# Kernel tuning notes

Hardware: AMD Instinct MI355X
Metric: run time of the kernel (lower is better)

## Reference

```python
import jax, jax.numpy as jnp
import numpy as np

NUM_HEADS = 4
WS = 3


def setup_inputs() -> dict:
    key = jax.random.key(0)
    k1, k2, k3 = jax.random.split(key, 3)
    B, Hs, Ws_, C = 16, 96, 96, 256
    x = jax.random.normal(k1, (B, Hs * Ws_, C), dtype=jnp.float32)
    # torch nn.Linear weights: [out_features, in_features]
    Wqkv = jax.random.normal(k2, (3 * C, C), dtype=jnp.float32) * (1.0 / np.sqrt(C))
    Wproj = jax.random.normal(k3, (C, C), dtype=jnp.float32) * (1.0 / np.sqrt(C))
    return {"x": x, "Wqkv": Wqkv, "Wproj": Wproj, "H": Hs, "W": Ws_}


def reference(x, Wqkv, Wproj, H, W):
    B, N, C = x.shape
    ws = WS
    nh = NUM_HEADS
    hd = C // nh
    scale = hd ** -0.5

    pad_h = (ws - H % ws) % ws
    pad_w = (ws - W % ws) % ws
    xg = x.reshape(B, H, W, C)
    if pad_h > 0 or pad_w > 0:
        xg = jnp.pad(xg, ((0, 0), (0, pad_h), (0, pad_w), (0, 0)))
    H_pad, W_pad = H + pad_h, W + pad_w
    nWh, nWw = H_pad // ws, W_pad // ws
    Bw = B * nWh * nWw

    # window partition: [B, nWh, ws, nWw, ws, C] -> [Bw, ws*ws, C]
    xw = xg.reshape(B, nWh, ws, nWw, ws, C).transpose(0, 1, 3, 2, 4, 5)
    xw = xw.reshape(Bw, ws * ws, C)

    # qkv projection (Linear, no bias): x @ W^T
    qkv = xw @ Wqkv.T                                   # [Bw, 9, 3C]
    qkv = qkv.reshape(Bw, ws * ws, 3, nh, hd).transpose(2, 0, 3, 1, 4)
    q, k, v = qkv[0], qkv[1], qkv[2]                    # [Bw, nh, 9, hd]

    attn = jnp.einsum("bhqd,bhkd->bhqk", q, k) * scale  # [Bw, nh, 9, 9]
    attn = jax.nn.softmax(attn, axis=-1)
    out = jnp.einsum("bhqk,bhkd->bhqd", attn, v)        # [Bw, nh, 9, hd]
    out = out.transpose(0, 2, 1, 3).reshape(Bw, ws * ws, C)
    out = out @ Wproj.T

    # window unpartition
    out = out.reshape(B, nWh, nWw, ws, ws, C).transpose(0, 1, 3, 2, 4, 5)
    out = out.reshape(B, H_pad, W_pad, C)
    if pad_h > 0 or pad_w > 0:
        out = out[:, :H, :W, :]
    return out.reshape(B, H * W, C)
```

## Files before the change

### kernel.cpp

```cpp
#include <hip/hip_runtime.h>
#include <hip/hip_bf16.h>

using f32x4  = __attribute__((ext_vector_type(4))) float;
using bf16x8 = __attribute__((ext_vector_type(8))) short;
using bf16x4 = __attribute__((ext_vector_type(4))) short;
using u32x2  = __attribute__((ext_vector_type(2))) unsigned int;
using u32x4  = __attribute__((ext_vector_type(4))) unsigned int;

__device__ __forceinline__ float bf2f(short s) {
    unsigned u = ((unsigned)(unsigned short)s) << 16;
    return __builtin_bit_cast(float, u);
}
__device__ __forceinline__ unsigned short f2b(float f) {
    unsigned u = __builtin_bit_cast(unsigned, f);
    unsigned r = u + 0x7FFFu + ((u >> 16) & 1u);
    return (unsigned short)(r >> 16);
}
__device__ __forceinline__ short f2b_hw(float f) {
    __hip_bfloat16 h = __float2bfloat16(f);
    return *reinterpret_cast<short*>(&h);
}
__device__ __forceinline__ void gl_lds16(const void* g, void* l) {
    __builtin_amdgcn_global_load_lds((const __attribute__((address_space(1))) void*)g,
                                     (__attribute__((address_space(3))) void*)l, 16, 0, 0);
}

__global__ void k_wconv(const float* __restrict__ wq, const float* __restrict__ wp,
                        unsigned short* __restrict__ out) {
    int i = blockIdx.x * 256 + threadIdx.x;
    float v = (i < 196608) ? wq[i] : wp[i - 196608];
    out[i] = f2b(v);
}

__global__ __launch_bounds__(256, 4) void k_qkv8(
    const float* __restrict__ x,
    const unsigned short* __restrict__ wqkv,
    unsigned short* __restrict__ qkv)
{
    __shared__ unsigned short As[128 * 64];
    __shared__ unsigned short Bs[128 * 64];
    const int tid = threadIdx.x;
    const int wv = tid >> 6, ln = tid & 63;
    const int lr = ln & 15, lk = ln >> 4;
    const int l8 = ln >> 3, c8 = ln & 7;

    const int b = blockIdx.x;
    const int xcd = b & 7, local = b >> 3;
    const int strip = local / 144, r = local % 144;
    const int n0 = (r / 24) * 128;
    const size_t m0 = (size_t)(xcd * 144 + strip * 24 + (r % 24)) * 128;
    const int mq = (wv >> 1) * 64, nq = (wv & 1) * 64;

    f32x4 acc[4][4];
#pragma unroll
    for (int mi = 0; mi < 4; ++mi)
#pragma unroll
        for (int ni = 0; ni < 4; ++ni) {
            f32x4 z = {0.f, 0.f, 0.f, 0.f};
            acc[mi][ni] = z;
        }

#pragma unroll 1
    for (int ks = 0; ks < 4; ++ks) {
        const int k0 = ks * 64;
        __syncthreads();
#pragma unroll
        for (int i = 0; i < 4; ++i) {
            int r8 = i * 8 + l8;
            int sc = (c8 ^ (r8 & 7)) * 8;
            gl_lds16(wqkv + (size_t)(n0 + wv * 32 + r8) * 256 + k0 + sc,
                     &Bs[(wv * 32 + i * 8) * 64]);
        }
#pragma unroll
        for (int i = 0; i < 4; ++i) {
            int slot = tid + 256 * i;
            int row = slot >> 3, ch = slot & 7;
            const f32x4* p = (const f32x4*)(x + (m0 + row) * 256 + k0 + ch * 8);
            f32x4 f0 = p[0], f1 = p[1];
            bf16x8 v;
#pragma unroll
            for (int j = 0; j < 4; ++j) {
                v[j]     = f2b_hw(f0[j]);
                v[4 + j] = f2b_hw(f1[j]);
            }
            *(bf16x8*)&As[row * 64 + ((ch ^ (row & 7)) * 8)] = v;
        }
        __syncthreads();

#pragma unroll
        for (int kk = 0; kk < 2; ++kk) {
            bf16x8 av[4], bv[4];
#pragma unroll
            for (int i = 0; i < 4; ++i) {
                int ar = mq + i * 16 + lr;
                av[i] = *(const bf16x8*)&As[ar * 64 + (((kk * 4 + lk) ^ (ar & 7)) * 8)];
                int br = nq + i * 16 + lr;
                bv[i] = *(const bf16x8*)&Bs[br * 64 + (((kk * 4 + lk) ^ (br & 7)) * 8)];
            }
#pragma unroll
            for (int mi = 0; mi < 4; ++mi)
#pragma unroll
                for (int ni = 0; ni < 4; ++ni)
                    acc[mi][ni] = __builtin_amdgcn_mfma_f32_16x16x32_bf16(bv[ni], av[mi], acc[mi][ni], 0, 0, 0);
        }
    }

#pragma unroll
    for (int mi = 0; mi < 4; ++mi) {
        const size_t row = m0 + mq + mi * 16 + lr;
#pragma unroll
        for (int ni = 0; ni < 4; ++ni) {
            u32x2 u;
            u[0] = (unsigned)f2b(acc[mi][ni][0]) | ((unsigned)f2b(acc[mi][ni][1]) << 16);
            u[1] = (unsigned)f2b(acc[mi][ni][2]) | ((unsigned)f2b(acc[mi][ni][3]) << 16);
            *(u32x2*)(qkv + row * 768 + n0 + nq + ni * 16 + lk * 4) = u;
        }
    }
}

__global__ __launch_bounds__(256) void k_attn(
    unsigned short* __restrict__ qkv)
{
    constexpr int LQ = 68;
    __shared__ unsigned short Ks[144 * LQ];
    __shared__ unsigned short Vs[144 * LQ];
    const int tid = threadIdx.x;
    const int t3 = blockIdx.x;
    const int hf = blockIdx.y;
    const int h  = blockIdx.z;
    const int bb = t3 >> 5, wh = t3 & 31;

    for (int idx = tid; idx < 1152; idx += 256) {
        int row = idx >> 3, ch = idx & 7;
        int ww = row / 9, t = row - ww * 9;
        int rr = t / 3, cc = t - rr * 3;
        size_t xrow = (size_t)bb * 9216 + (wh * 3 + rr) * 96 + hf * 48 + ww * 3 + cc;
        *(bf16x8*)&Ks[row * LQ + ch * 8] = *(const bf16x8*)(qkv + xrow * 768 + 256 + h * 64 + ch * 8);
        *(bf16x8*)&Vs[row * LQ + ch * 8] = *(const bf16x8*)(qkv + xrow * 768 + 512 + h * 64 + ch * 8);
    }
    __syncthreads();

#pragma unroll 1
    for (int pass = 0; pass < 2; ++pass) {
        int row;
        bool act;
        if (pass == 0) { row = tid >> 1;            act = true; }
        else           { row = 128 + (tid >> 1);    act = tid < 32; }
        if (act) {
            const int hc = tid & 1;
            const int w9 = (row / 9) * 9;
            int t = row - w9;
            int rr = t / 3, cc = t - rr * 3;
            size_t xrow = (size_t)bb * 9216 + (wh * 3 + rr) * 96 + hf * 48 + (w9 / 9) * 3 + cc;
            unsigned short* qp = qkv + xrow * 768 + h * 64 + hc * 32;
            float q[32];
#pragma unroll
            for (int g = 0; g < 4; ++g) {
                bf16x8 v = *(const bf16x8*)(qp + g * 8);
#pragma unroll
                for (int j = 0; j < 8; ++j) q[g * 8 + j] = bf2f(v[j]);
            }
            float s[9];
#pragma unroll
            for (int kk = 0; kk < 9; ++kk) {
                float acc = 0.f;
#pragma unroll
                for (int g = 0; g < 4; ++g) {
                    bf16x8 v = *(const bf16x8*)&Ks[(w9 + kk) * LQ + hc * 32 + g * 8];
#pragma unroll
                    for (int j = 0; j < 8; ++j) acc += q[g * 8 + j] * bf2f(v[j]);
                }
                s[kk] = acc;
            }
#pragma unroll
            for (int kk = 0; kk < 9; ++kk)
                s[kk] = (s[kk] + __shfl_xor(s[kk], 1)) * 0.125f;
            float m = s[0];
#pragma unroll
            for (int kk = 1; kk < 9; ++kk) m = fmaxf(m, s[kk]);
            float sum = 0.f;
#pragma unroll
            for (int kk = 0; kk < 9; ++kk) { s[kk] = __expf(s[kk] - m); sum += s[kk]; }
            float inv = 1.f / sum;
            float o[32];
#pragma unroll
            for (int d = 0; d < 32; ++d) o[d] = 0.f;
#pragma unroll
            for (int kk = 0; kk < 9; ++kk) {
                float pk = s[kk] * inv;
#pragma unroll
                for (int g = 0; g < 4; ++g) {
                    bf16x8 v = *(const bf16x8*)&Vs[(w9 + kk) * LQ + hc * 32 + g * 8];
#pragma unroll
                    for (int j = 0; j < 8; ++j) o[g * 8 + j] += pk * bf2f(v[j]);
                }
            }
#pragma unroll
            for (int grp = 0; grp < 4; ++grp) {
                u32x4 u;
#pragma unroll
                for (int e = 0; e < 4; ++e) {
                    int i0 = grp * 8 + e * 2;
                    u[e] = (unsigned)f2b(o[i0]) | ((unsigned)f2b(o[i0 + 1]) << 16);
                }
                *(u32x4*)(qp + grp * 8) = u;
            }
        }
    }
}

__global__ __launch_bounds__(256) void k_proj(
    const unsigned short* __restrict__ ain,
    const unsigned short* __restrict__ wproj,
    float* __restrict__ out)
{
    __shared__ unsigned short As[128 * 64];
    __shared__ unsigned short Bs[128 * 64];
    const int tid = threadIdx.x;
    const int wv = tid >> 6, ln = tid & 63;
    const int lr = ln & 15, lk = ln >> 4;
    const int l8 = ln >> 3, c8 = ln & 7;

    int b = blockIdx.x;
    int w = (b & 7) * 288 + (b >> 3);
    const size_t m0 = (size_t)(w >> 1) * 128;
    const int n0 = (w & 1) * 128;
    const int mq = (wv >> 1) * 64, nq = (wv & 1) * 64;

    f32x4 acc[4][4];
#pragma unroll
    for (int mi = 0; mi < 4; ++mi)
#pragma unroll
        for (int ni = 0; ni < 4; ++ni) {
            f32x4 z = {0.f, 0.f, 0.f, 0.f};
            acc[mi][ni] = z;
        }

#pragma unroll 1
    for (int ks = 0; ks < 4; ++ks) {
        const int k0 = ks * 64;
        __syncthreads();
#pragma unroll
        for (int i = 0; i < 4; ++i) {
            int r8 = i * 8 + l8;
            int sc = (c8 ^ (r8 & 7)) * 8;
            gl_lds16(ain   + (m0 + wv * 32 + r8) * 768 + k0 + sc,
                     &As[(wv * 32 + i * 8) * 64]);
            gl_lds16(wproj + (size_t)(n0 + wv * 32 + r8) * 256 + k0 + sc,
                     &Bs[(wv * 32 + i * 8) * 64]);
        }
        __syncthreads();

#pragma unroll
        for (int kk = 0; kk < 2; ++kk) {
            bf16x8 av[4], bv[4];
#pragma unroll
            for (int i = 0; i < 4; ++i) {
                int ar = mq + i * 16 + lr;
                av[i] = *(const bf16x8*)&As[ar * 64 + (((kk * 4 + lk) ^ (ar & 7)) * 8)];
                int br = nq + i * 16 + lr;
                bv[i] = *(const bf16x8*)&Bs[br * 64 + (((kk * 4 + lk) ^ (br & 7)) * 8)];
            }
#pragma unroll
            for (int mi = 0; mi < 4; ++mi)
#pragma unroll
                for (int ni = 0; ni < 4; ++ni)
                    acc[mi][ni] = __builtin_amdgcn_mfma_f32_16x16x32_bf16(bv[ni], av[mi], acc[mi][ni], 0, 0, 0);
        }
    }

#pragma unroll
    for (int mi = 0; mi < 4; ++mi) {
        const size_t row = m0 + mq + mi * 16 + lr;
#pragma unroll
        for (int ni = 0; ni < 4; ++ni)
            *(f32x4*)&out[row * 256 + n0 + nq + ni * 16 + lk * 4] = acc[mi][ni];
    }
}


__device__ __forceinline__ int grow_of(int wbase, int row) {
    int wi = row / 9;
    int t  = row - wi * 9;
    int w  = wbase + wi;
    if (w >= 16384) return -1;
    int b = w >> 10, rem = w & 1023;
    int wh = rem >> 5, ww = rem & 31;
    int r = t / 3, c = t - r * 3;
    return b * 9216 + (wh * 3 + r) * 96 + ww * 3 + c;
}

__global__ __launch_bounds__(256) void k_winattn_fb(
    const float* __restrict__ x,
    const unsigned short* __restrict__ wqkv,
    unsigned short* __restrict__ aout)
{
    constexpr int LDA = 264;
    constexpr int LQ  = 68;
    __shared__ unsigned short As[64 * LDA];
    __shared__ unsigned short Qb[3][64 * LQ];
    __shared__ int rowmap[64];

    const int tid = threadIdx.x;
    const int wbase = blockIdx.x * 7;
    const int wv = tid >> 6, ln = tid & 63;
    const int lr = ln & 15, lk = ln >> 4;
    const int mw = wv >> 1, nw = wv & 1;

    if (tid < 64)
        rowmap[tid] = (tid < 63) ? grow_of(wbase, tid) : -1;
    __syncthreads();

    for (int idx = tid; idx < 64 * 32; idx += 256) {
        int row = idx >> 5, g = idx & 31;
        int gr = rowmap[row];
        bf16x8 v;
        if (gr >= 0) {
            const f32x4* p = (const f32x4*)(x + (size_t)gr * 256 + g * 8);
            f32x4 f0 = p[0], f1 = p[1];
#pragma unroll
            for (int j = 0; j < 4; ++j) {
                v[j]     = (short)f2b(f0[j]);
                v[4 + j] = (short)f2b(f1[j]);
            }
        } else {
#pragma unroll
            for (int j = 0; j < 8; ++j) v[j] = 0;
        }
        *(bf16x8*)&As[row * LDA + g * 8] = v;
    }
    __syncthreads();

#pragma unroll 1
    for (int h = 0; h < 4; ++h) {
#pragma unroll 1
        for (int part = 0; part < 3; ++part) {
            const int j0 = part * 256 + h * 64 + nw * 32;
            bf16x8 w[2][8];
#pragma unroll
            for (int ni = 0; ni < 2; ++ni)
#pragma unroll
                for (int kk = 0; kk < 8; ++kk)
                    w[ni][kk] = *(const bf16x8*)(wqkv + (size_t)(j0 + ni * 16 + lr) * 256 + kk * 32 + lk * 8);

            f32x4 acc[2][2];
#pragma unroll
            for (int mi = 0; mi < 2; ++mi)
#pragma unroll
                for (int ni = 0; ni < 2; ++ni) {
                    f32x4 z = {0.f, 0.f, 0.f, 0.f};
                    acc[mi][ni] = z;
                }
#pragma unroll
            for (int kk = 0; kk < 8; ++kk) {
                const int k0 = kk * 32 + lk * 8;
                bf16x8 a0 = *(const bf16x8*)&As[(mw * 32 + lr) * LDA + k0];
                bf16x8 a1 = *(const bf16x8*)&As[(mw * 32 + 16 + lr) * LDA + k0];
                acc[0][0] = __builtin_amdgcn_mfma_f32_16x16x32_bf16(w[0][kk], a0, acc[0][0], 0, 0, 0);
                acc[1][0] = __builtin_amdgcn_mfma_f32_16x16x32_bf16(w[0][kk], a1, acc[1][0], 0, 0, 0);
                acc[0][1] = __builtin_amdgcn_mfma_f32_16x16x32_bf16(w[1][kk], a0, acc[0][1], 0, 0, 0);
                acc[1][1] = __builtin_amdgcn_mfma_f32_16x16x32_bf16(w[1][kk], a1, acc[1][1], 0, 0, 0);
            }
#pragma unroll
            for (int mi = 0; mi < 2; ++mi)
#pragma unroll
                for (int ni = 0; ni < 2; ++ni) {
                    int row = mw * 32 + mi * 16 + lr;
                    int col = nw * 32 + ni * 16 + lk * 4;
                    u32x2 u;
                    u[0] = (unsigned)f2b(acc[mi][ni][0]) | ((unsigned)f2b(acc[mi][ni][1]) << 16);
                    u[1] = (unsigned)f2b(acc[mi][ni][2]) | ((unsigned)f2b(acc[mi][ni][3]) << 16);
                    *(u32x2*)&Qb[part][row * LQ + col] = u;
                }
        }
        __syncthreads();
        {
            const int row = wv * 16 + lr;
            const int c   = lk;
            if (row < 63) {
                const int w9 = (row / 9) * 9;
                float q[16];
#pragma unroll
                for (int g = 0; g < 4; ++g) {
                    bf16x4 v = *(const bf16x4*)&Qb[0][row * LQ + c * 16 + g * 4];
#pragma unroll
                    for (int j = 0; j < 4; ++j) q[g * 4 + j] = bf2f(v[j]);
                }
                float s[9];
#pragma unroll
                for (int kk = 0; kk < 9; ++kk) {
                    float t = 0.f;
#pragma unroll
                    for (int g = 0; g < 4; ++g) {
                        bf16x4 v = *(const bf16x4*)&Qb[1][(w9 + kk) * LQ + c * 16 + g * 4];
#pragma unroll
                        for (int j = 0; j < 4; ++j) t += q[g * 4 + j] * bf2f(v[j]);
                    }
                    s[kk] = t;
                }
#pragma unroll
                for (int kk = 0; kk < 9; ++kk) {
                    float t = s[kk];
                    t += __shfl_xor(t, 16);
                    t += __shfl_xor(t, 32);
                    s[kk] = t * 0.125f;
                }
                float m = s[0];
#pragma unroll
                for (int kk = 1; kk < 9; ++kk) m = fmaxf(m, s[kk]);
                float sum = 0.f;
#pragma unroll
                for (int kk = 0; kk < 9; ++kk) { s[kk] = __expf(s[kk] - m); sum += s[kk]; }
                float inv = 1.f / sum;
                float o[16];
#pragma unroll
                for (int d = 0; d < 16; ++d) o[d] = 0.f;
#pragma unroll
                for (int kk = 0; kk < 9; ++kk) {
                    float pk = s[kk] * inv;
#pragma unroll
                    for (int g = 0; g < 4; ++g) {
                        bf16x4 v = *(const bf16x4*)&Qb[2][(w9 + kk) * LQ + c * 16 + g * 4];
#pragma unroll
                        for (int j = 0; j < 4; ++j) o[g * 4 + j] += pk * bf2f(v[j]);
                    }
                }
                const int gr = rowmap[row];
                if (gr >= 0) {
#pragma unroll
                    for (int half = 0; half < 2; ++half) {
                        u32x4 u;
#pragma unroll
                        for (int e = 0; e < 4; ++e) {
                            int i0 = half * 8 + e * 2;
                            u[e] = (unsigned)f2b(o[i0]) | ((unsigned)f2b(o[i0 + 1]) << 16);
                        }
                        *(u32x4*)(aout + (size_t)gr * 256 + h * 64 + c * 16 + half * 8) = u;
                    }
                }
            }
        }
        __syncthreads();
    }
}

__global__ __launch_bounds__(256) void k_proj_fb(
    const unsigned short* __restrict__ ain,
    const unsigned short* __restrict__ wproj,
    float* __restrict__ out)
{
    const int tid = threadIdx.x;
    const int wv = tid >> 6, ln = tid & 63;
    const int lr = ln & 15, lk = ln >> 4;
    const size_t row0 = (size_t)blockIdx.x * 128;

    bf16x8 af[2][8];
#pragma unroll
    for (int mi = 0; mi < 2; ++mi) {
        const size_t row = row0 + wv * 32 + mi * 16 + lr;
#pragma unroll
        for (int kk = 0; kk < 8; ++kk)
            af[mi][kk] = *(const bf16x8*)(ain + row * 256 + kk * 32 + lk * 8);
    }
#pragma unroll
    for (int nc = 0; nc < 4; ++nc) {
        const int j0 = nc * 64;
        f32x4 acc[2][4];
#pragma unroll
        for (int mi = 0; mi < 2; ++mi)
#pragma unroll
            for (int ni = 0; ni < 4; ++ni) {
                f32x4 z = {0.f, 0.f, 0.f, 0.f};
                acc[mi][ni] = z;
            }
#pragma unroll
        for (int kk = 0; kk < 8; ++kk) {
            bf16x8 w[4];
#pragma unroll
            for (int ni = 0; ni < 4; ++ni)
                w[ni] = *(const bf16x8*)(wproj + (size_t)(j0 + ni * 16 + lr) * 256 + kk * 32 + lk * 8);
#pragma unroll
            for (int ni = 0; ni < 4; ++ni) {
                acc[0][ni] = __builtin_amdgcn_mfma_f32_16x16x32_bf16(w[ni], af[0][kk], acc[0][ni], 0, 0, 0);
                acc[1][ni] = __builtin_amdgcn_mfma_f32_16x16x32_bf16(w[ni], af[1][kk], acc[1][ni], 0, 0, 0);
            }
        }
#pragma unroll
        for (int mi = 0; mi < 2; ++mi) {
            const size_t row = row0 + wv * 32 + mi * 16 + lr;
#pragma unroll
            for (int ni = 0; ni < 4; ++ni)
                *(f32x4*)&out[row * 256 + j0 + ni * 16 + lk * 4] = acc[mi][ni];
        }
    }
}

extern "C" void kernel_launch(void* const* d_in, const int* in_sizes, int n_in,
                              void* d_out, int out_size, void* d_ws, size_t ws_size,
                              hipStream_t stream) {
    const float* x  = (const float*)d_in[0];
    const float* wq = (const float*)d_in[1];
    const float* wp = (const float*)d_in[2];
    unsigned short* wsb     = (unsigned short*)d_ws;
    unsigned short* wqkv_b  = wsb;
    unsigned short* wproj_b = wsb + 196608;
    float* out = (float*)d_out;

    k_wconv<<<1024, 256, 0, stream>>>(wq, wp, wsb);

    const size_t need = 524288ULL + 147456ULL * 768ULL * 2ULL;
    if (ws_size >= need) {
        unsigned short* qkv = wsb + 262144;
        k_qkv8<<<6912, 256, 0, stream>>>(x, wqkv_b, qkv);
        k_attn<<<dim3(512, 2, 4), 256, 0, stream>>>(qkv);
        k_proj<<<2304, 256, 0, stream>>>(qkv, wproj_b, out);
    } else {
        unsigned short* aout = wsb + 262144;
        k_winattn_fb<<<2341, 256, 0, stream>>>(x, wqkv_b, aout);
        k_proj_fb  <<<1152, 256, 0, stream>>>(aout, wproj_b, out);
    }
}
```

Measured before the change: 275.1 us.

## Keep x row tile in registers and sweep all QKV output columns per block

The QKV GEMM now has each block own 64 rows of x. It converts those rows to bf16 once and holds them in registers as MFMA fragments. The block then loops over all six 128-column chunks of Wqkv, staging weight tiles through LDS. Previously, x (fp32, the largest input) was re-read and re-converted for each of the six N tiles. The costs are a large register footprint with no occupancy hint, serialized N chunks inside each block, and more barriers per block.

New measurement: 458.1 us. +66.5%, slower.

```diff
diff --git a/kernel.cpp b/kernel.cpp
--- a/kernel.cpp
+++ b/kernel.cpp
@@ -32,50 +32,26 @@
     out[i] = f2b(v);
 }
 
-__global__ __launch_bounds__(256, 4) void k_qkv8(
+__global__ __launch_bounds__(256) void k_qkv11(
     const float* __restrict__ x,
     const unsigned short* __restrict__ wqkv,
     unsigned short* __restrict__ qkv)
 {
-    __shared__ unsigned short As[128 * 64];
-    __shared__ unsigned short Bs[128 * 64];
+    __shared__ unsigned short Bs[128 * 128];
     const int tid = threadIdx.x;
     const int wv = tid >> 6, ln = tid & 63;
     const int lr = ln & 15, lk = ln >> 4;
-    const int l8 = ln >> 3, c8 = ln & 7;
-
-    const int b = blockIdx.x;
-    const int xcd = b & 7, local = b >> 3;
-    const int strip = local / 144, r = local % 144;
-    const int n0 = (r / 24) * 128;
-    const size_t m0 = (size_t)(xcd * 144 + strip * 24 + (r % 24)) * 128;
-    const int mq = (wv >> 1) * 64, nq = (wv & 1) * 64;
-
-    f32x4 acc[4][4];
-#pragma unroll
-    for (int mi = 0; mi < 4; ++mi)
-#pragma unroll
-        for (int ni = 0; ni < 4; ++ni) {
-            f32x4 z = {0.f, 0.f, 0.f, 0.f};
-            acc[mi][ni] = z;
-        }
-
-#pragma unroll 1
-    for (int ks = 0; ks < 4; ++ks) {
-        const int k0 = ks * 64;
-        __syncthreads();
-#pragma unroll
-        for (int i = 0; i < 4; ++i) {
-            int r8 = i * 8 + l8;
-            int sc = (c8 ^ (r8 & 7)) * 8;
-            gl_lds16(wqkv + (size_t)(n0 + wv * 32 + r8) * 256 + k0 + sc,
-                     &Bs[(wv * 32 + i * 8) * 64]);
-        }
-#pragma unroll
-        for (int i = 0; i < 4; ++i) {
-            int slot = tid + 256 * i;
-            int row = slot >> 3, ch = slot & 7;
-            const f32x4* p = (const f32x4*)(x + (m0 + row) * 256 + k0 + ch * 8);
+
+    const size_t m0 = (size_t)blockIdx.x * 64;
+    const int mq = (wv >> 1) * 32, nq = (wv & 1) * 64;
+
+    bf16x8 af[2][8];
+#pragma unroll
+    for (int mi = 0; mi < 2; ++mi) {
+        const float* xp = x + (m0 + mq + mi * 16 + lr) * 256;
+#pragma unroll
+        for (int ks = 0; ks < 8; ++ks) {
+            const f32x4* p = (const f32x4*)(xp + ks * 32 + lk * 8);
             f32x4 f0 = p[0], f1 = p[1];
             bf16x8 v;
 #pragma unroll
@@ -83,37 +59,61 @@
                 v[j]     = f2b_hw(f0[j]);
                 v[4 + j] = f2b_hw(f1[j]);
             }
-            *(bf16x8*)&As[row * 64 + ((ch ^ (row & 7)) * 8)] = v;
-        }
-        __syncthreads();
-
-#pragma unroll
-        for (int kk = 0; kk < 2; ++kk) {
-            bf16x8 av[4], bv[4];
-#pragma unroll
-            for (int i = 0; i < 4; ++i) {
-                int ar = mq + i * 16 + lr;
-                av[i] = *(const bf16x8*)&As[ar * 64 + (((kk * 4 + lk) ^ (ar & 7)) * 8)];
-                int br = nq + i * 16 + lr;
-                bv[i] = *(const bf16x8*)&Bs[br * 64 + (((kk * 4 + lk) ^ (br & 7)) * 8)];
-            }
-#pragma unroll
-            for (int mi = 0; mi < 4; ++mi)
-#pragma unroll
-                for (int ni = 0; ni < 4; ++ni)
-                    acc[mi][ni] = __builtin_amdgcn_mfma_f32_16x16x32_bf16(bv[ni], av[mi], acc[mi][ni], 0, 0, 0);
-        }
-    }
-
-#pragma unroll
-    for (int mi = 0; mi < 4; ++mi) {
-        const size_t row = m0 + mq + mi * 16 + lr;
-#pragma unroll
-        for (int ni = 0; ni < 4; ++ni) {
-            u32x2 u;
-            u[0] = (unsigned)f2b(acc[mi][ni][0]) | ((unsigned)f2b(acc[mi][ni][1]) << 16);
-            u[1] = (unsigned)f2b(acc[mi][ni][2]) | ((unsigned)f2b(acc[mi][ni][3]) << 16);
-            *(u32x2*)(qkv + row * 768 + n0 + nq + ni * 16 + lk * 4) = u;
+            af[mi][ks] = v;
+        }
+    }
+
+#pragma unroll 1
+    for (int nc = 0; nc < 6; ++nc) {
+        const int n0 = nc * 128;
+        f32x4 acc[2][4];
+#pragma unroll
+        for (int mi = 0; mi < 2; ++mi)
+#pragma unroll
+            for (int ni = 0; ni < 4; ++ni) {
+                f32x4 z = {0.f, 0.f, 0.f, 0.f};
+                acc[mi][ni] = z;
+            }
+
+#pragma unroll 1
+        for (int ph = 0; ph < 2; ++ph) {
+            __syncthreads();
+#pragma unroll
+            for (int i = 0; i < 8; ++i) {
+                int rr = wv * 32 + i * 4 + (ln >> 4);
+                int sc = ((ln & 15) ^ (rr & 15)) * 8;
+                gl_lds16(wqkv + (size_t)(n0 + rr) * 256 + ph * 128 + sc,
+                         &Bs[(wv * 32 + i * 4) * 128]);
+            }
+            __syncthreads();
+
+#pragma unroll
+            for (int kk = 0; kk < 4; ++kk) {
+                bf16x8 bv[4];
+#pragma unroll
+                for (int ni = 0; ni < 4; ++ni) {
+                    int br = nq + ni * 16 + lr;
+                    bv[ni] = *(const bf16x8*)&Bs[br * 128 + (((kk * 4 + lk) ^ (br & 15)) * 8)];
+                }
+#pragma unroll
+                for (int mi = 0; mi < 2; ++mi)
+#pragma unroll
+                    for (int ni = 0; ni < 4; ++ni)
+                        acc[mi][ni] = __builtin_amdgcn_mfma_f32_16x16x32_bf16(
+                            bv[ni], af[mi][ph * 4 + kk], acc[mi][ni], 0, 0, 0);
+            }
+        }
+
+#pragma unroll
+        for (int mi = 0; mi < 2; ++mi) {
+            const size_t row = m0 + mq + mi * 16 + lr;
+#pragma unroll
+            for (int ni = 0; ni < 4; ++ni) {
+                u32x2 u;
+                u[0] = (unsigned)f2b(acc[mi][ni][0]) | ((unsigned)f2b(acc[mi][ni][1]) << 16);
+                u[1] = (unsigned)f2b(acc[mi][ni][2]) | ((unsigned)f2b(acc[mi][ni][3]) << 16);
+                *(u32x2*)(qkv + row * 768 + n0 + nq + ni * 16 + lk * 4) = u;
+            }
         }
     }
 }
@@ -511,9 +511,9 @@
     const size_t need = 524288ULL + 147456ULL * 768ULL * 2ULL;
     if (ws_size >= need) {
         unsigned short* qkv = wsb + 262144;
-        k_qkv8<<<6912, 256, 0, stream>>>(x, wqkv_b, qkv);
-        k_attn<<<dim3(512, 2, 4), 256, 0, stream>>>(qkv);
-        k_proj<<<2304, 256, 0, stream>>>(qkv, wproj_b, out);
+        k_qkv11<<<2304, 256, 0, stream>>>(x, wqkv_b, qkv);
+        k_attn <<<dim3(512, 2, 4), 256, 0, stream>>>(qkv);
+        k_proj <<<2304, 256, 0, stream>>>(qkv, wproj_b, out);
     } else {
         unsigned short* aout = wsb + 262144;
         k_winattn_fb<<<2341, 256, 0, stream>>>(x, wqkv_b, aout);
```
